# Kernel optimization log

Hardware: AMD Instinct MI355X
Metric: run time of the kernel (lower is better)

The kernel has to match this reference:

```python
import jax, jax.numpy as jnp
import numpy as np

H, S, B, R, IN, NN, OP = 512, 256, 32, 16, 4, 16, 6
NEG = -1.0e12


def setup_inputs() -> dict:
    key = jax.random.key(0)
    ks = jax.random.split(key, 40)
    f32 = jnp.float32
    inp = {}
    inp["node_emb"] = jax.random.normal(ks[0], (B, 1, H), f32)
    inp["left"] = jax.random.normal(ks[1], (B, 1, H), f32)
    inp["encoder_outputs"] = jax.random.normal(ks[2], (S, B, H), f32)
    inp["num_pades"] = jax.random.normal(ks[3], (B, NN, H), f32)
    inp["formula_scores"] = jax.random.normal(ks[4], (R, H), f32)
    inp["has_left"] = jax.random.bernoulli(ks[5], 0.5, (B,))
    lengths = jax.random.randint(ks[6], (B,), S // 2, S + 1)
    inp["seq_mask"] = jnp.arange(S)[None, :] >= lengths[:, None]
    nlen = jax.random.randint(ks[7], (B,), (IN + NN) // 2, IN + NN + 1)
    inp["mask_nums"] = jnp.arange(IN + NN)[None, :] >= nlen[:, None]
    sc = 0.04  # init scale for weights
    def w(i, shape):
        return jax.random.normal(ks[i], shape, f32) * sc
    inp["embedding_weight"] = jax.random.normal(ks[8], (1, IN, H), f32)
    inp["Wcl"] = w(9, (H, H));    inp["bcl"] = jnp.zeros((H,), f32)
    inp["Wclg"] = w(10, (H, H));  inp["bclg"] = jnp.zeros((H,), f32)
    inp["Wcr"] = w(11, (2 * H, H));  inp["bcr"] = jnp.zeros((H,), f32)
    inp["Wcrg"] = w(12, (2 * H, H)); inp["bcrg"] = jnp.zeros((H,), f32)
    inp["Wops"] = w(13, (2 * H, OP)); inp["bops"] = jnp.zeros((OP,), f32)
    inp["Wattn"] = w(14, (2 * H, H)); inp["battn"] = jnp.zeros((H,), f32)
    inp["wattn_s"] = w(15, (H,));     inp["battn_s"] = jnp.zeros((), f32)
    inp["Wfattn"] = w(16, (2 * H, H)); inp["bfattn"] = jnp.zeros((H,), f32)
    inp["wfattn_s"] = w(17, (H,));     inp["bfattn_s"] = jnp.zeros((), f32)
    inp["Wscore"] = w(18, (3 * H, H)); inp["bscore"] = jnp.zeros((H,), f32)
    inp["wscore_s"] = w(19, (H,))  # Score.score has no bias
    inp["Wfp1"] = w(20, (H, H));   inp["bfp1"] = jnp.zeros((H,), f32)
    inp["Wfp2"] = w(21, (H,));     inp["bfp2"] = jnp.zeros((), f32)
    return inp


def _forward(node_emb, left, has_left, encoder_outputs, num_pades, seq_mask,
             mask_nums, formula_scores, embedding_weight, Wcl, bcl, Wclg, bclg,
             Wcr, bcr, Wcrg, bcrg, Wops, bops, Wattn, battn, wattn_s, battn_s,
             Wfattn, bfattn, wfattn_s, bfattn_s, Wscore, bscore, wscore_s,
             Wfp1, bfp1, Wfp2, bfp2):
    # gated left/right node update (dropout = identity, eval mode)
    c = node_emb                                            # [B,1,H]
    lc = jnp.concatenate([left, c], axis=-1)                # [B,1,2H]
    out_l = jnp.tanh(c @ Wcl + bcl) * jax.nn.sigmoid(c @ Wclg + bclg)
    out_r = jnp.tanh(lc @ Wcr + bcr) * jax.nn.sigmoid(lc @ Wcrg + bcrg)
    current_node = jnp.where(has_left[:, None, None], out_r, out_l)  # [B,1,H]
    # TreeAttn(current_node, encoder_outputs): additive attention over S
    Wh, We = Wattn[:H], Wattn[H:]
    feat = jnp.tanh(current_node[:, 0][None] @ Wh + encoder_outputs @ We + battn)  # [S,B,H]
    en = (feat @ wattn_s + battn_s).T                       # [B,S]
    en = jnp.where(seq_mask, NEG, en)
    current_attn = jax.nn.softmax(en, axis=1)[:, None, :]   # [B,1,S]
    eo_b = jnp.transpose(encoder_outputs, (1, 0, 2))        # [B,S,H]
    current_context = current_attn @ eo_b                   # [B,1,H]
    # embedding table = learned constants + numbers from the problem
    emb_w = jnp.concatenate(
        [jnp.broadcast_to(embedding_weight, (node_emb.shape[0], IN, H)), num_pades], axis=1)  # [B,IN+NN,H]
    leaf_input = jnp.concatenate([current_node, current_context], axis=2)[:, 0]  # [B,2H]
    # FormulaAttn: additive attention of each formula over all tokens
    Wfe, Wff = Wfattn[:H], Wfattn[H:]
    ffeat = jnp.tanh(encoder_outputs[None] @ Wfe
                     + (formula_scores @ Wff)[:, None, None, :] + bfattn)  # [R,S,B,H]
    fen = jnp.transpose(ffeat @ wfattn_s + bfattn_s, (2, 0, 1))            # [B,R,S]
    fen = jnp.where(seq_mask[:, None, :], NEG, fen)
    formulas_attn = jax.nn.softmax(fen, axis=-1)            # [B,R,S]
    formulas_context = (formulas_attn + 0.2 * current_attn) @ eo_b         # [B,R,H]
    formula_feat = jnp.tanh(formulas_context @ Wfp1 + bfp1)
    formula_prob = jax.nn.softmax(formula_feat @ Wfp2 + bfp2, axis=-1)     # [B,R]
    # Score over candidate number embeddings
    N = IN + NN
    hid = jnp.broadcast_to(leaf_input[:, None, :], (leaf_input.shape[0], N, 2 * H))
    ein = jnp.concatenate([hid, emb_w], axis=-1)            # [B,N,3H]
    ns = jnp.tanh(ein @ Wscore + bscore) @ wscore_s         # [B,N]
    num_score = jnp.where(mask_nums, NEG, ns)
    op = leaf_input @ Wops + bops                           # [B,OP]
    return (num_score, op, current_node, current_context, emb_w, formula_prob)


def reference(node_emb, left, has_left, encoder_outputs, num_pades, seq_mask,
              mask_nums, formula_scores, embedding_weight, Wcl, bcl, Wclg, bclg,
              Wcr, bcr, Wcrg, bcrg, Wops, bops, Wattn, battn, wattn_s, battn_s,
              Wfattn, bfattn, wfattn_s, bfattn_s, Wscore, bscore, wscore_s,
              Wfp1, bfp1, Wfp2, bfp2):
    return _forward(node_emb, left, has_left, encoder_outputs, num_pades,
                    seq_mask, mask_nums, formula_scores, embedding_weight,
                    Wcl, bcl, Wclg, bclg, Wcr, bcr, Wcrg, bcrg, Wops, bops,
                    Wattn, battn, wattn_s, battn_s, Wfattn, bfattn, wfattn_s,
                    bfattn_s, Wscore, bscore, wscore_s, Wfp1, bfp1, Wfp2, bfp2)
```

## Files before the change

### kernel.cpp

```cpp
#include <hip/hip_runtime.h>
#include <hip/hip_bf16.h>
#include <stdint.h>

#define H 512
#define S 256
#define B 32
#define R 16
#define NEG -1000000000000.0f

typedef unsigned short u16;
typedef short short8 __attribute__((ext_vector_type(8)));
typedef float f32x4 __attribute__((ext_vector_type(4)));

__device__ __forceinline__ float bf2f(u16 u) {
  unsigned int v = ((unsigned int)u) << 16;
  float f; __builtin_memcpy(&f, &v, 4); return f;
}
__device__ __forceinline__ u16 f2u(float x) {
  __hip_bfloat16 h = __float2bfloat16(x);
  u16 u; __builtin_memcpy(&u, &h, 2); return u;
}
__device__ __forceinline__ float ftanh(float x) {
  float e = __expf(2.f * x);
  return 1.f - 2.f * __builtin_amdgcn_rcpf(e + 1.f);
}
__device__ __forceinline__ float fsig(float x) {
  return __builtin_amdgcn_rcpf(1.f + __expf(-x));
}
__device__ __forceinline__ void gload16(const void* g, void* l) {
  __builtin_amdgcn_global_load_lds(
      (const __attribute__((address_space(1))) unsigned int*)g,
      (__attribute__((address_space(3))) unsigned int*)l, 16, 0, 0);
}

__device__ __forceinline__ void trans_tile(const float* __restrict__ src, int nb, int k0,
                                           u16* __restrict__ dst, int n0, int Krows,
                                           float (*tile)[65], int t) {
  #pragma unroll
  for (int it = 0; it < 16; ++it) {
    int f = it * 256 + t; int r = f >> 6, c = f & 63;
    tile[r][c] = src[(size_t)(k0 + r) * 512 + nb + c];
  }
  __syncthreads();
  #pragma unroll
  for (int it = 0; it < 16; ++it) {
    int f = it * 256 + t; int r = f >> 6, c = f & 63;
    dst[(size_t)(n0 + r) * Krows + k0 + c] = f2u(tile[c][r]);
  }
}

__global__ __launch_bounds__(256) void k_prep1(
    const float* __restrict__ enc, u16* __restrict__ encb,
    const float* __restrict__ Wattn, const float* __restrict__ Wfattn, u16* __restrict__ Wt,
    const float* __restrict__ Wscore, u16* __restrict__ Wt2f,
    const float* __restrict__ Wfp1, u16* __restrict__ Wt3,
    const float* __restrict__ node_emb, const float* __restrict__ left,
    const int* __restrict__ has_left,
    const float* __restrict__ Wcl, const float* __restrict__ Wclg,
    const float* __restrict__ Wcr, const float* __restrict__ Wcrg,
    const float* __restrict__ fs,
    float* __restrict__ gp1, float* __restrict__ gp2, float* __restrict__ cwp,
    const float* __restrict__ emb_w, const float* __restrict__ num_pades,
    float* __restrict__ out_embw, u16* __restrict__ einb) {
  __shared__ float tile[64][65];
  __shared__ float x[128];
  int id = blockIdx.x, t = threadIdx.x;
  if (id < 2048) {
    int i = (id * 256 + t) * 8;
    float4 a = *(const float4*)(enc + i);
    float4 b = *(const float4*)(enc + i + 4);
    short8 o;
    o[0] = (short)f2u(a.x); o[1] = (short)f2u(a.y); o[2] = (short)f2u(a.z); o[3] = (short)f2u(a.w);
    o[4] = (short)f2u(b.x); o[5] = (short)f2u(b.y); o[6] = (short)f2u(b.z); o[7] = (short)f2u(b.w);
    *(short8*)(encb + i) = o;
  } else if (id < 2176) {
    int f = id - 2048; int gx = f & 15, gy = f >> 4;
    int n0 = gx * 64, k0 = gy * 64;
    const float* src = (n0 < 512) ? (Wattn + 512 * 512) : Wfattn;
    int nb = (n0 < 512) ? n0 : n0 - 512;
    trans_tile(src, nb, k0, Wt, n0, 512, tile, t);
  } else if (id < 2368) {
    int f = id - 2176; int gx = f & 7, gy = f >> 3;
    trans_tile(Wscore, gx * 64, gy * 64, Wt2f, gx * 64, 1536, tile, t);
  } else if (id < 2432) {
    int f = id - 2368; int gx = f & 7, gy = f >> 3;
    trans_tile(Wfp1, gx * 64, gy * 64, Wt3, gx * 64, 512, tile, t);
  } else if (id < 2688) {
    int f = id - 2432;
    int b = f >> 3, kc = f & 7;
    int hl = has_left[b];
    int k0 = kc * 128;
    float* o1 = gp1 + ((size_t)b * 8 + kc) * 512;
    float* o2 = gp2 + ((size_t)b * 8 + kc) * 512;
    if (!hl && kc >= 4) { o1[t] = 0.f; o1[t + 256] = 0.f; o2[t] = 0.f; o2[t + 256] = 0.f; return; }
    if (t < 128) {
      int k = k0 + t;
      x[t] = hl ? (k < 512 ? left[b * 512 + k] : node_emb[b * 512 + k - 512])
                : node_emb[b * 512 + k];
    }
    __syncthreads();
    const float* W1 = hl ? Wcr : Wcl;
    const float* W2 = hl ? Wcrg : Wclg;
    float a1 = 0.f, a2 = 0.f, a3 = 0.f, a4 = 0.f;
    for (int kk = 0; kk < 128; ++kk) {
      float xv = x[kk];
      const float* w1r = W1 + (size_t)(k0 + kk) * 512;
      const float* w2r = W2 + (size_t)(k0 + kk) * 512;
      a1 += xv * w1r[t]; a2 += xv * w1r[t + 256];
      a3 += xv * w2r[t]; a4 += xv * w2r[t + 256];
    }
    o1[t] = a1; o1[t + 256] = a2; o2[t] = a3; o2[t + 256] = a4;
  } else if (id < 2752) {
    int f = id - 2688; int row = f >> 2, kc = f & 3;
    int k0 = kc * 128;
    if (t < 128) x[t] = fs[row * 512 + k0 + t];
    __syncthreads();
    const float* W = Wfattn + (size_t)(512 + k0) * 512;
    float a1 = 0.f, a2 = 0.f;
    for (int kk = 0; kk < 128; ++kk) {
      float xv = x[kk];
      a1 += xv * W[(size_t)kk * 512 + t];
      a2 += xv * W[(size_t)kk * 512 + t + 256];
    }
    float* o = cwp + ((size_t)(32 + row) * 4 + kc) * 512;
    o[t] = a1; o[t + 256] = a2;
  } else {
    int f = id - 2752;
    #pragma unroll
    for (int rr = 0; rr < 2; ++rr) {
      int row = f * 2 + rr;
      int n = row % 20, b = row / 20;
      #pragma unroll
      for (int i = 0; i < 2; ++i) {
        int h = t + 256 * i;
        float v = (n < 4) ? emb_w[n * 512 + h] : num_pades[((size_t)b * 16 + n - 4) * 512 + h];
        out_embw[(size_t)row * 512 + h] = v;
        einb[(size_t)row * 1536 + 1024 + h] = f2u(v);
      }
    }
  }
}

template <int FM, int FN, bool OUT16>
__device__ __forceinline__ void gemm_body(
    const u16* __restrict__ A, const u16* __restrict__ Bt,
    u16* __restrict__ C16, float* __restrict__ C32,
    int lda, int ldb, int ldc, int ksteps,
    int bm, int bn, int kbase, long zoff,
    u16* As, u16* Bs) {
  constexpr int BM = FM * 32, BN = FN * 32;
  const int tid = threadIdx.x;
  const int lane = tid & 63;
  const int wid = tid >> 6;
  const int wr = (wid >> 1) * (FM * 16);
  const int wc = (wid & 1) * (FN * 16);
  f32x4 acc[FM][FN];
  #pragma unroll
  for (int m = 0; m < FM; ++m)
    #pragma unroll
    for (int n = 0; n < FN; ++n)
      #pragma unroll
      for (int q = 0; q < 4; ++q) acc[m][n][q] = 0.f;

  const int kb = (lane >> 4) * 8;
  const int rr = lane & 15;
  for (int ks = 0; ks < ksteps; ++ks) {
    int k0 = kbase + ks * 32;
    #pragma unroll
    for (int it = 0; it < BM / 64; ++it) {
      int c = it * 256 + tid;
      gload16(A + (size_t)(bm + (c >> 2)) * lda + k0 + (c & 3) * 8, As + c * 8);
    }
    #pragma unroll
    for (int it = 0; it < BN / 64; ++it) {
      int c = it * 256 + tid;
      gload16(Bt + (size_t)(bn + (c >> 2)) * ldb + k0 + (c & 3) * 8, Bs + c * 8);
    }
    __syncthreads();
    short8 af[FM], bf[FN];
    #pragma unroll
    for (int m = 0; m < FM; ++m)
      af[m] = *(const short8*)(As + (wr + m * 16 + rr) * 32 + kb);
    #pragma unroll
    for (int n = 0; n < FN; ++n)
      bf[n] = *(const short8*)(Bs + (wc + n * 16 + rr) * 32 + kb);
    #pragma unroll
    for (int m = 0; m < FM; ++m)
      #pragma unroll
      for (int n = 0; n < FN; ++n)
        acc[m][n] = __builtin_amdgcn_mfma_f32_16x16x32_bf16(af[m], bf[n], acc[m][n], 0, 0, 0);
    __syncthreads();
  }
  int r0 = (lane >> 4) * 4, cc = lane & 15;
  #pragma unroll
  for (int m = 0; m < FM; ++m)
    #pragma unroll
    for (int n = 0; n < FN; ++n)
      #pragma unroll
      for (int q = 0; q < 4; ++q) {
        long row = bm + wr + m * 16 + r0 + q;
        long col = bn + wc + n * 16 + cc;
        if (OUT16) C16[zoff + row * ldc + col] = f2u(acc[m][n][q]);
        else       C32[zoff + row * ldc + col] = acc[m][n][q];
      }
}

__global__ __launch_bounds__(256) void k_g1(
    const u16* __restrict__ encb, const u16* __restrict__ Wt, u16* __restrict__ EW,
    const float* __restrict__ cwp, const float* __restrict__ battn,
    const float* __restrict__ bfattn, float* __restrict__ CW, float* __restrict__ FW) {
  __shared__ u16 As[128 * 32];
  __shared__ u16 Bs[128 * 32];
  if (blockIdx.y == 0 && blockIdx.x < 48) {
    int row = blockIdx.x, t = threadIdx.x;
    #pragma unroll
    for (int i = 0; i < 2; ++i) {
      int h = t + 256 * i;
      float s = cwp[((size_t)row * 4 + 0) * 512 + h] + cwp[((size_t)row * 4 + 1) * 512 + h] +
                cwp[((size_t)row * 4 + 2) * 512 + h] + cwp[((size_t)row * 4 + 3) * 512 + h];
      if (row < 32) CW[row * 512 + h] = s + battn[h];
      else          FW[(row - 32) * 512 + h] = s + bfattn[h];
    }
  }
  gemm_body<4, 4, true>(encb, Wt, EW, nullptr, 512, 512, 1024, 16,
                        blockIdx.x * 128, blockIdx.y * 128, 0, 0, As, Bs);
}

__global__ __launch_bounds__(256) void k_tt(
    const u16* __restrict__ einb, const u16* __restrict__ Wt2f, float* __restrict__ Tp,
    const u16* __restrict__ fctxb, const u16* __restrict__ Wt3, float* __restrict__ T3p) {
  __shared__ u16 As[64 * 32];
  __shared__ u16 Bs[64 * 32];
  int q = blockIdx.x;
  if (q < 320) {
    int x = q % 10, y = (q / 10) % 8, z = q / 80;
    gemm_body<2, 2, false>(einb, Wt2f, nullptr, Tp, 1536, 1536, 512, 12,
                           x * 64, y * 64, z * 12 * 32, (long)z * 327680, As, Bs);
  } else {
    int q2 = q - 320;
    int x = q2 % 8, y = (q2 / 8) % 8, z = q2 / 64;
    gemm_body<2, 2, false>(fctxb, Wt3, nullptr, T3p, 512, 512, 512, 8,
                           x * 64, y * 64, z * 8 * 32, (long)z * 262144, As, Bs);
  }
}

__global__ __launch_bounds__(256) void k_p2(
    const float* __restrict__ gp1, const float* __restrict__ gp2,
    const int* __restrict__ has_left,
    const float* __restrict__ bcl, const float* __restrict__ bclg,
    const float* __restrict__ bcr, const float* __restrict__ bcrg,
    const float* __restrict__ Wattn,
    float* __restrict__ cur_node, float* __restrict__ out_cn, float* __restrict__ cwp) {
  int id = blockIdx.x, t = threadIdx.x;
  int row = id >> 2, kc = id & 3;
  int k0 = kc * 128;
  __shared__ float x[128];
  int hl = has_left[row];
  if (t < 128) {
    int h = k0 + t;
    float s1 = 0.f, s2 = 0.f;
    #pragma unroll
    for (int c = 0; c < 8; ++c) {
      s1 += gp1[((size_t)row * 8 + c) * 512 + h];
      s2 += gp2[((size_t)row * 8 + c) * 512 + h];
    }
    float v = ftanh(s1 + (hl ? bcr[h] : bcl[h])) * fsig(s2 + (hl ? bcrg[h] : bclg[h]));
    x[t] = v;
    cur_node[row * 512 + h] = v;
    out_cn[row * 512 + h] = v;
  }
  __syncthreads();
  const float* W = Wattn + (size_t)k0 * 512;
  float a1 = 0.f, a2 = 0.f;
  for (int kk = 0; kk < 128; ++kk) {
    float xv = x[kk];
    a1 += xv * W[(size_t)kk * 512 + t];
    a2 += xv * W[(size_t)kk * 512 + t + 256];
  }
  float* o = cwp + ((size_t)row * 4 + kc) * 512;
  o[t] = a1; o[t + 256] = a2;
}

__global__ __launch_bounds__(256) void k_enfen(
    const u16* __restrict__ EW, const float* __restrict__ CW,
    const float* __restrict__ FW,
    const float* __restrict__ wattn_s, const float* __restrict__ battn_s,
    const float* __restrict__ wfattn_s, const float* __restrict__ bfattn_s,
    const int* __restrict__ seq_mask, float* __restrict__ en, float* __restrict__ fen) {
  __shared__ float sFW[16 * 512];
  __shared__ float swf[512], swa[512], scw[512];
  int bid = blockIdx.x;
  int b = bid >> 6;
  int s0 = (bid & 63) * 4;
  int t = threadIdx.x;
  #pragma unroll
  for (int q = 0; q < 32; ++q) sFW[q * 256 + t] = FW[q * 256 + t];
  swf[t] = wfattn_s[t]; swf[256 + t] = wfattn_s[256 + t];
  swa[t] = wattn_s[t];  swa[256 + t] = wattn_s[256 + t];
  scw[t] = CW[b * 512 + t]; scw[256 + t] = CW[b * 512 + 256 + t];
  __syncthreads();
  int w = t >> 6, lane = t & 63;
  int s = s0 + w;
  const u16* ew = EW + (size_t)(s * 32 + b) * 1024;
  float ewf[8], wfv[8];
  float accE = 0.f;
  #pragma unroll
  for (int i = 0; i < 8; ++i) {
    int h = lane + 64 * i;
    accE += ftanh(scw[h] + bf2f(ew[h])) * swa[h];
    ewf[i] = bf2f(ew[512 + h]);
    wfv[i] = swf[h];
  }
  for (int o = 32; o >= 1; o >>= 1) accE += __shfl_down(accE, o);
  int msk = seq_mask[b * 256 + s];
  if (lane == 0) en[b * 256 + s] = msk ? NEG : (accE + battn_s[0]);
  for (int r = 0; r < 16; ++r) {
    float a = 0.f;
    #pragma unroll
    for (int i = 0; i < 8; ++i) {
      int h = lane + 64 * i;
      a += ftanh(sFW[r * 512 + h] + ewf[i]) * wfv[i];
    }
    for (int o = 32; o >= 1; o >>= 1) a += __shfl_down(a, o);
    if (lane == 0) fen[((size_t)b * 16 + r) * 256 + s] = msk ? NEG : (a + bfattn_s[0]);
  }
}

__global__ __launch_bounds__(512) void k_ctxall(
    const float* __restrict__ en, const float* __restrict__ fen,
    const u16* __restrict__ encb, const float* __restrict__ cur_node,
    float* __restrict__ out_ctx, float* __restrict__ leaf, u16* __restrict__ fctxb,
    u16* __restrict__ einb) {
  int br = blockIdx.x;
  int b = br / 17, j = br % 17;
  int t = threadIdx.x;
  __shared__ float red[512];
  __shared__ float sa[256];
  float xe = (t < 256) ? en[b * 256 + t] : NEG;
  red[t] = xe; __syncthreads();
  for (int o = 256; o > 0; o >>= 1) { if (t < o) red[t] = fmaxf(red[t], red[t + o]); __syncthreads(); }
  float m = red[0]; __syncthreads();
  float ee = (t < 256) ? __expf(xe - m) : 0.f;
  red[t] = ee; __syncthreads();
  for (int o = 256; o > 0; o >>= 1) { if (t < o) red[t] += red[t + o]; __syncthreads(); }
  float attn_v = ee / red[0];
  __syncthreads();
  float coef = attn_v;
  if (j < 16) {
    float xf = (t < 256) ? fen[((size_t)b * 16 + j) * 256 + t] : NEG;
    red[t] = xf; __syncthreads();
    for (int o = 256; o > 0; o >>= 1) { if (t < o) red[t] = fmaxf(red[t], red[t + o]); __syncthreads(); }
    float mf = red[0]; __syncthreads();
    float ef = (t < 256) ? __expf(xf - mf) : 0.f;
    red[t] = ef; __syncthreads();
    for (int o = 256; o > 0; o >>= 1) { if (t < o) red[t] += red[t + o]; __syncthreads(); }
    coef = ef / red[0] + 0.2f * attn_v;
    __syncthreads();
  }
  if (t < 256) sa[t] = coef;
  __syncthreads();
  int h = t;
  float acc = 0.f;
  for (int s = 0; s < 256; ++s)
    acc += sa[s] * bf2f(encb[((size_t)s * 32 + b) * 512 + h]);
  if (j < 16) {
    fctxb[((size_t)b * 16 + j) * 512 + h] = f2u(acc);
  } else {
    float cn = cur_node[b * 512 + h];
    out_ctx[b * 512 + h] = acc;
    leaf[b * 1024 + 512 + h] = acc;
    leaf[b * 1024 + h] = cn;
    u16 v1 = f2u(cn), v2 = f2u(acc);
    for (int n = 0; n < 20; ++n) {
      einb[(size_t)(b * 20 + n) * 1536 + h] = v1;
      einb[(size_t)(b * 20 + n) * 1536 + 512 + h] = v2;
    }
  }
}

__global__ __launch_bounds__(256) void k_epi(
    const float* __restrict__ Tp, const float* __restrict__ bscore,
    const float* __restrict__ wscore_s, const int* __restrict__ mask_nums,
    float* __restrict__ out_ns,
    const float* __restrict__ T3p, const float* __restrict__ bfp1,
    const float* __restrict__ Wfp2, const float* __restrict__ bfp2,
    float* __restrict__ out_fp,
    const float* __restrict__ leaf, const float* __restrict__ Wops,
    const float* __restrict__ bops, float* __restrict__ out_op) {
  int id = blockIdx.x, t = threadIdx.x;
  int w = t >> 6, lane = t & 63;
  __shared__ float red[16];
  if (id < 640) {
    int row = id;
    float acc = 0.f;
    #pragma unroll
    for (int i = 0; i < 2; ++i) {
      int h = t + 256 * i;
      float tv = Tp[(size_t)row * 512 + h] + Tp[327680 + (size_t)row * 512 + h] +
                 Tp[2L * 327680 + (size_t)row * 512 + h] + Tp[3L * 327680 + (size_t)row * 512 + h] +
                 bscore[h];
      acc += ftanh(tv) * wscore_s[h];
    }
    for (int o = 32; o >= 1; o >>= 1) acc += __shfl_down(acc, o);
    if (lane == 0) red[w] = acc;
    __syncthreads();
    if (t == 0) out_ns[row] = mask_nums[row] ? NEG : (red[0] + red[1] + red[2] + red[3]);
  } else if (id < 672) {
    int b = id - 640;
    #pragma unroll
    for (int j2 = 0; j2 < 4; ++j2) {
      int j = w * 4 + j2;
      int row = b * 16 + j;
      float acc = 0.f;
      #pragma unroll
      for (int i = 0; i < 8; ++i) {
        int h = lane + 64 * i;
        float v = T3p[(size_t)row * 512 + h] + T3p[262144 + (size_t)row * 512 + h] + bfp1[h];
        acc += ftanh(v) * Wfp2[h];
      }
      for (int o = 32; o >= 1; o >>= 1) acc += __shfl_down(acc, o);
      if (lane == 0) red[j] = acc + bfp2[0];
    }
    __syncthreads();
    if (t < 16) {
      float xx = red[t];
      float mm = xx;
      for (int o = 8; o >= 1; o >>= 1) mm = fmaxf(mm, __shfl_xor(mm, o, 16));
      float e = __expf(xx - mm);
      float s2 = e;
      for (int o = 8; o >= 1; o >>= 1) s2 += __shfl_xor(s2, o, 16);
      out_fp[b * 16 + t] = e / s2;
    }
  } else {
    int f = id - 672; int o = f % 6, b = f / 6;
    float acc = 0.f;
    #pragma unroll
    for (int i = 0; i < 4; ++i) {
      int k = t + 256 * i;
      acc += leaf[b * 1024 + k] * Wops[(size_t)k * 6 + o];
    }
    for (int off = 32; off >= 1; off >>= 1) acc += __shfl_down(acc, off);
    if (lane == 0) red[w] = acc;
    __syncthreads();
    if (t == 0) out_op[b * 6 + o] = red[0] + red[1] + red[2] + red[3] + bops[o];
  }
}

extern "C" void kernel_launch(void* const* d_in, const int* in_sizes, int n_in,
                              void* d_out, int out_size, void* d_ws, size_t ws_size,
                              hipStream_t stream) {
  const float* node_emb  = (const float*)d_in[0];
  const float* left      = (const float*)d_in[1];
  const float* enc       = (const float*)d_in[2];
  const float* num_pades = (const float*)d_in[3];
  const float* fs        = (const float*)d_in[4];
  const int*   has_left  = (const int*)d_in[5];
  const int*   seq_mask  = (const int*)d_in[6];
  const int*   mask_nums = (const int*)d_in[7];
  const float* emb_w     = (const float*)d_in[8];
  const float* Wcl  = (const float*)d_in[9];
  const float* bcl  = (const float*)d_in[10];
  const float* Wclg = (const float*)d_in[11];
  const float* bclg = (const float*)d_in[12];
  const float* Wcr  = (const float*)d_in[13];
  const float* bcr  = (const float*)d_in[14];
  const float* Wcrg = (const float*)d_in[15];
  const float* bcrg = (const float*)d_in[16];
  const float* Wops = (const float*)d_in[17];
  const float* bops = (const float*)d_in[18];
  const float* Wattn   = (const float*)d_in[19];
  const float* battn   = (const float*)d_in[20];
  const float* wattn_s = (const float*)d_in[21];
  const float* battn_s = (const float*)d_in[22];
  const float* Wfattn   = (const float*)d_in[23];
  const float* bfattn   = (const float*)d_in[24];
  const float* wfattn_s = (const float*)d_in[25];
  const float* bfattn_s = (const float*)d_in[26];
  const float* Wscore   = (const float*)d_in[27];
  const float* bscore   = (const float*)d_in[28];
  const float* wscore_s = (const float*)d_in[29];
  const float* Wfp1 = (const float*)d_in[30];
  const float* bfp1 = (const float*)d_in[31];
  const float* Wfp2 = (const float*)d_in[32];
  const float* bfp2 = (const float*)d_in[33];

  float* out = (float*)d_out;
  float* out_ns   = out + 0;
  float* out_op   = out + 640;
  float* out_cn   = out + 832;
  float* out_ctx  = out + 17216;
  float* out_embw = out + 33600;
  float* out_fp   = out + 361280;

  uint8_t* wsb = (uint8_t*)d_ws;
  u16*   encb = (u16*)(wsb + 0);
  u16*   Wt   = (u16*)(wsb + 8388608);
  u16*   Wt2f = (u16*)(wsb + 9437184);
  u16*   Wt3  = (u16*)(wsb + 11010048);
  u16*   EW   = (u16*)(wsb + 11534336);
  u16*   einb = (u16*)(wsb + 28311552);
  float* Tp   = (float*)(wsb + 30277632);
  float* T3p  = (float*)(wsb + 35520512);
  float* fb   = (float*)(wsb + 37617664);
  float* cur_node = fb + 0;
  float* CW   = fb + 16384;
  float* FW   = fb + 32768;
  float* en   = fb + 40960;
  float* fen  = fb + 49152;
  float* leaf = fb + 180224;
  u16*   fctxb= (u16*)(fb + 212992);
  float* gp1  = fb + 344064;
  float* gp2  = fb + 475136;
  float* cwp  = fb + 606208;

  k_prep1<<<3072, 256, 0, stream>>>(enc, encb, Wattn, Wfattn, Wt, Wscore, Wt2f, Wfp1, Wt3,
                                    node_emb, left, has_left, Wcl, Wclg, Wcr, Wcrg, fs,
                                    gp1, gp2, cwp, emb_w, num_pades, out_embw, einb);
  k_p2<<<128, 256, 0, stream>>>(gp1, gp2, has_left, bcl, bclg, bcr, bcrg, Wattn,
                                cur_node, out_cn, cwp);
  k_g1<<<dim3(64, 8), 256, 0, stream>>>(encb, Wt, EW, cwp, battn, bfattn, CW, FW);
  k_enfen<<<2048, 256, 0, stream>>>(EW, CW, FW, wattn_s, battn_s, wfattn_s, bfattn_s, seq_mask, en, fen);
  k_ctxall<<<544, 512, 0, stream>>>(en, fen, encb, cur_node, out_ctx, leaf, fctxb, einb);
  k_tt<<<448, 256, 0, stream>>>(einb, Wt2f, Tp, fctxb, Wt3, T3p);
  k_epi<<<864, 256, 0, stream>>>(Tp, bscore, wscore_s, mask_nums, out_ns,
                                 T3p, bfp1, Wfp2, bfp2, out_fp,
                                 leaf, Wops, bops, out_op);
}
```

Before: 118.0 us.

## Move attention projections into MFMA GEMM and deepen split-K for score GEMMs

The current_node@Wattn and formula_scores@Wfattn projections, previously scalar fp32 matvecs in k_prep1/k_p2, are now a bf16 MFMA GEMM tile added to k_g1 using a newly transposed weight Wt4. Biases are folded into k_enfen. The split-K factor of the k_tt GEMMs doubles to raise block count, and the epilogue sums more partials. It also unrolls the context loop. The cost is an extra weight transpose, more partial-sum traffic, and bf16 rounding of the projection inputs.

```diff
diff --git a/kernel.cpp b/kernel.cpp
--- a/kernel.cpp
+++ b/kernel.cpp
@@ -54,12 +54,12 @@
     const float* __restrict__ Wattn, const float* __restrict__ Wfattn, u16* __restrict__ Wt,
     const float* __restrict__ Wscore, u16* __restrict__ Wt2f,
     const float* __restrict__ Wfp1, u16* __restrict__ Wt3,
+    u16* __restrict__ Wt4,
     const float* __restrict__ node_emb, const float* __restrict__ left,
     const int* __restrict__ has_left,
     const float* __restrict__ Wcl, const float* __restrict__ Wclg,
     const float* __restrict__ Wcr, const float* __restrict__ Wcrg,
-    const float* __restrict__ fs,
-    float* __restrict__ gp1, float* __restrict__ gp2, float* __restrict__ cwp,
+    float* __restrict__ gp1, float* __restrict__ gp2,
     const float* __restrict__ emb_w, const float* __restrict__ num_pades,
     float* __restrict__ out_embw, u16* __restrict__ einb) {
   __shared__ float tile[64][65];
@@ -85,8 +85,14 @@
   } else if (id < 2432) {
     int f = id - 2368; int gx = f & 7, gy = f >> 3;
     trans_tile(Wfp1, gx * 64, gy * 64, Wt3, gx * 64, 512, tile, t);
-  } else if (id < 2688) {
-    int f = id - 2432;
+  } else if (id < 2560) {
+    int f = id - 2432; int gx = f & 15, gy = f >> 4;
+    int n0 = gx * 64, k0 = gy * 64;
+    const float* src = (n0 < 512) ? Wattn : (Wfattn + 512 * 512);
+    int nb = (n0 < 512) ? n0 : n0 - 512;
+    trans_tile(src, nb, k0, Wt4, n0, 512, tile, t);
+  } else if (id < 2816) {
+    int f = id - 2560;
     int b = f >> 3, kc = f & 7;
     int hl = has_left[b];
     int k0 = kc * 128;
@@ -110,22 +116,8 @@
       a3 += xv * w2r[t]; a4 += xv * w2r[t + 256];
     }
     o1[t] = a1; o1[t + 256] = a2; o2[t] = a3; o2[t + 256] = a4;
-  } else if (id < 2752) {
-    int f = id - 2688; int row = f >> 2, kc = f & 3;
-    int k0 = kc * 128;
-    if (t < 128) x[t] = fs[row * 512 + k0 + t];
-    __syncthreads();
-    const float* W = Wfattn + (size_t)(512 + k0) * 512;
-    float a1 = 0.f, a2 = 0.f;
-    for (int kk = 0; kk < 128; ++kk) {
-      float xv = x[kk];
-      a1 += xv * W[(size_t)kk * 512 + t];
-      a2 += xv * W[(size_t)kk * 512 + t + 256];
-    }
-    float* o = cwp + ((size_t)(32 + row) * 4 + kc) * 512;
-    o[t] = a1; o[t + 256] = a2;
   } else {
-    int f = id - 2752;
+    int f = id - 2816;
     #pragma unroll
     for (int rr = 0; rr < 2; ++rr) {
       int row = f * 2 + rr;
@@ -141,7 +133,7 @@
   }
 }
 
-template <int FM, int FN, bool OUT16>
+template <int FM, int FN>
 __device__ __forceinline__ void gemm_body(
     const u16* __restrict__ A, const u16* __restrict__ Bt,
     u16* __restrict__ C16, float* __restrict__ C32,
@@ -200,30 +192,21 @@
       for (int q = 0; q < 4; ++q) {
         long row = bm + wr + m * 16 + r0 + q;
         long col = bn + wc + n * 16 + cc;
-        if (OUT16) C16[zoff + row * ldc + col] = f2u(acc[m][n][q]);
-        else       C32[zoff + row * ldc + col] = acc[m][n][q];
+        if (C16) C16[zoff + row * ldc + col] = f2u(acc[m][n][q]);
+        else     C32[zoff + row * ldc + col] = acc[m][n][q];
       }
 }
 
 __global__ __launch_bounds__(256) void k_g1(
     const u16* __restrict__ encb, const u16* __restrict__ Wt, u16* __restrict__ EW,
-    const float* __restrict__ cwp, const float* __restrict__ battn,
-    const float* __restrict__ bfattn, float* __restrict__ CW, float* __restrict__ FW) {
+    const u16* __restrict__ cnfs, const u16* __restrict__ Wt4, float* __restrict__ CWFW) {
   __shared__ u16 As[128 * 32];
   __shared__ u16 Bs[128 * 32];
-  if (blockIdx.y == 0 && blockIdx.x < 48) {
-    int row = blockIdx.x, t = threadIdx.x;
-    #pragma unroll
-    for (int i = 0; i < 2; ++i) {
-      int h = t + 256 * i;
-      float s = cwp[((size_t)row * 4 + 0) * 512 + h] + cwp[((size_t)row * 4 + 1) * 512 + h] +
-                cwp[((size_t)row * 4 + 2) * 512 + h] + cwp[((size_t)row * 4 + 3) * 512 + h];
-      if (row < 32) CW[row * 512 + h] = s + battn[h];
-      else          FW[(row - 32) * 512 + h] = s + bfattn[h];
-    }
-  }
-  gemm_body<4, 4, true>(encb, Wt, EW, nullptr, 512, 512, 1024, 16,
-                        blockIdx.x * 128, blockIdx.y * 128, 0, 0, As, Bs);
+  int x = blockIdx.x, y = blockIdx.y;
+  if (x < 64)
+    gemm_body<4, 4>(encb, Wt, EW, nullptr, 512, 512, 1024, 16, x * 128, y * 128, 0, 0, As, Bs);
+  else
+    gemm_body<4, 4>(cnfs, Wt4, nullptr, CWFW, 512, 512, 1024, 16, 0, y * 128, 0, 0, As, Bs);
 }
 
 __global__ __launch_bounds__(256) void k_tt(
@@ -232,15 +215,15 @@
   __shared__ u16 As[64 * 32];
   __shared__ u16 Bs[64 * 32];
   int q = blockIdx.x;
-  if (q < 320) {
+  if (q < 640) {
     int x = q % 10, y = (q / 10) % 8, z = q / 80;
-    gemm_body<2, 2, false>(einb, Wt2f, nullptr, Tp, 1536, 1536, 512, 12,
-                           x * 64, y * 64, z * 12 * 32, (long)z * 327680, As, Bs);
+    gemm_body<2, 2>(einb, Wt2f, nullptr, Tp, 1536, 1536, 512, 6,
+                    x * 64, y * 64, z * 6 * 32, (long)z * 327680, As, Bs);
   } else {
-    int q2 = q - 320;
+    int q2 = q - 640;
     int x = q2 % 8, y = (q2 / 8) % 8, z = q2 / 64;
-    gemm_body<2, 2, false>(fctxb, Wt3, nullptr, T3p, 512, 512, 512, 8,
-                           x * 64, y * 64, z * 8 * 32, (long)z * 262144, As, Bs);
+    gemm_body<2, 2>(fctxb, Wt3, nullptr, T3p, 512, 512, 512, 4,
+                    x * 64, y * 64, z * 4 * 32, (long)z * 262144, As, Bs);
   }
 }
 
@@ -249,41 +232,41 @@
     const int* __restrict__ has_left,
     const float* __restrict__ bcl, const float* __restrict__ bclg,
     const float* __restrict__ bcr, const float* __restrict__ bcrg,
-    const float* __restrict__ Wattn,
-    float* __restrict__ cur_node, float* __restrict__ out_cn, float* __restrict__ cwp) {
+    const float* __restrict__ fs,
+    float* __restrict__ cur_node, float* __restrict__ out_cn, u16* __restrict__ cnfs) {
   int id = blockIdx.x, t = threadIdx.x;
-  int row = id >> 2, kc = id & 3;
-  int k0 = kc * 128;
-  __shared__ float x[128];
-  int hl = has_left[row];
-  if (t < 128) {
-    int h = k0 + t;
-    float s1 = 0.f, s2 = 0.f;
-    #pragma unroll
-    for (int c = 0; c < 8; ++c) {
-      s1 += gp1[((size_t)row * 8 + c) * 512 + h];
-      s2 += gp2[((size_t)row * 8 + c) * 512 + h];
-    }
-    float v = ftanh(s1 + (hl ? bcr[h] : bcl[h])) * fsig(s2 + (hl ? bcrg[h] : bclg[h]));
-    x[t] = v;
-    cur_node[row * 512 + h] = v;
-    out_cn[row * 512 + h] = v;
-  }
-  __syncthreads();
-  const float* W = Wattn + (size_t)k0 * 512;
-  float a1 = 0.f, a2 = 0.f;
-  for (int kk = 0; kk < 128; ++kk) {
-    float xv = x[kk];
-    a1 += xv * W[(size_t)kk * 512 + t];
-    a2 += xv * W[(size_t)kk * 512 + t + 256];
-  }
-  float* o = cwp + ((size_t)row * 4 + kc) * 512;
-  o[t] = a1; o[t + 256] = a2;
+  if (id < 32) {
+    int b = id, hl = has_left[b];
+    #pragma unroll
+    for (int i = 0; i < 2; ++i) {
+      int h = t + 256 * i;
+      float s1 = 0.f, s2 = 0.f;
+      #pragma unroll
+      for (int c = 0; c < 8; ++c) {
+        s1 += gp1[((size_t)b * 8 + c) * 512 + h];
+        s2 += gp2[((size_t)b * 8 + c) * 512 + h];
+      }
+      float v = ftanh(s1 + (hl ? bcr[h] : bcl[h])) * fsig(s2 + (hl ? bcrg[h] : bclg[h]));
+      cur_node[b * 512 + h] = v;
+      out_cn[b * 512 + h] = v;
+      cnfs[b * 512 + h] = f2u(v);
+    }
+  } else if (id < 48) {
+    int r = id - 32;
+    #pragma unroll
+    for (int i = 0; i < 2; ++i) {
+      int h = t + 256 * i;
+      cnfs[id * 512 + h] = f2u(fs[r * 512 + h]);
+    }
+  } else {
+    #pragma unroll
+    for (int i = 0; i < 2; ++i) cnfs[id * 512 + t + 256 * i] = 0;
+  }
 }
 
 __global__ __launch_bounds__(256) void k_enfen(
-    const u16* __restrict__ EW, const float* __restrict__ CW,
-    const float* __restrict__ FW,
+    const u16* __restrict__ EW, const float* __restrict__ CWFW,
+    const float* __restrict__ battn, const float* __restrict__ bfattn,
     const float* __restrict__ wattn_s, const float* __restrict__ battn_s,
     const float* __restrict__ wfattn_s, const float* __restrict__ bfattn_s,
     const int* __restrict__ seq_mask, float* __restrict__ en, float* __restrict__ fen) {
@@ -294,10 +277,15 @@
   int s0 = (bid & 63) * 4;
   int t = threadIdx.x;
   #pragma unroll
-  for (int q = 0; q < 32; ++q) sFW[q * 256 + t] = FW[q * 256 + t];
+  for (int q = 0; q < 32; ++q) {
+    int flat = q * 256 + t;
+    int r = flat >> 9, h = flat & 511;
+    sFW[flat] = CWFW[(size_t)(32 + r) * 1024 + 512 + h] + bfattn[h];
+  }
   swf[t] = wfattn_s[t]; swf[256 + t] = wfattn_s[256 + t];
   swa[t] = wattn_s[t];  swa[256 + t] = wattn_s[256 + t];
-  scw[t] = CW[b * 512 + t]; scw[256 + t] = CW[b * 512 + 256 + t];
+  scw[t] = CWFW[(size_t)b * 1024 + t] + battn[t];
+  scw[256 + t] = CWFW[(size_t)b * 1024 + 256 + t] + battn[256 + t];
   __syncthreads();
   int w = t >> 6, lane = t & 63;
   int s = s0 + w;
@@ -361,6 +349,7 @@
   __syncthreads();
   int h = t;
   float acc = 0.f;
+  #pragma unroll 8
   for (int s = 0; s < 256; ++s)
     acc += sa[s] * bf2f(encb[((size_t)s * 32 + b) * 512 + h]);
   if (j < 16) {
@@ -396,9 +385,9 @@
     #pragma unroll
     for (int i = 0; i < 2; ++i) {
       int h = t + 256 * i;
-      float tv = Tp[(size_t)row * 512 + h] + Tp[327680 + (size_t)row * 512 + h] +
-                 Tp[2L * 327680 + (size_t)row * 512 + h] + Tp[3L * 327680 + (size_t)row * 512 + h] +
-                 bscore[h];
+      float tv = bscore[h];
+      #pragma unroll
+      for (int z = 0; z < 8; ++z) tv += Tp[(size_t)z * 327680 + (size_t)row * 512 + h];
       acc += ftanh(tv) * wscore_s[h];
     }
     for (int o = 32; o >= 1; o >>= 1) acc += __shfl_down(acc, o);
@@ -415,7 +404,9 @@
       #pragma unroll
       for (int i = 0; i < 8; ++i) {
         int h = lane + 64 * i;
-        float v = T3p[(size_t)row * 512 + h] + T3p[262144 + (size_t)row * 512 + h] + bfp1[h];
+        float v = bfp1[h];
+        #pragma unroll
+        for (int z = 0; z < 4; ++z) v += T3p[(size_t)z * 262144 + (size_t)row * 512 + h];
         acc += ftanh(v) * Wfp2[h];
       }
       for (int o = 32; o >= 1; o >>= 1) acc += __shfl_down(acc, o);
@@ -497,31 +488,32 @@
   u16*   Wt   = (u16*)(wsb + 8388608);
   u16*   Wt2f = (u16*)(wsb + 9437184);
   u16*   Wt3  = (u16*)(wsb + 11010048);
-  u16*   EW   = (u16*)(wsb + 11534336);
-  u16*   einb = (u16*)(wsb + 28311552);
-  float* Tp   = (float*)(wsb + 30277632);
-  float* T3p  = (float*)(wsb + 35520512);
-  float* fb   = (float*)(wsb + 37617664);
+  u16*   Wt4  = (u16*)(wsb + 11534336);
+  u16*   EW   = (u16*)(wsb + 12582912);
+  u16*   einb = (u16*)(wsb + 29360128);
+  u16*   cnfs = (u16*)(wsb + 31326208);
+  float* CWFW = (float*)(wsb + 31457280);
+  float* Tp   = (float*)(wsb + 31981568);
+  float* T3p  = (float*)(wsb + 42467328);
+  float* fb   = (float*)(wsb + 46661632);
   float* cur_node = fb + 0;
-  float* CW   = fb + 16384;
-  float* FW   = fb + 32768;
-  float* en   = fb + 40960;
-  float* fen  = fb + 49152;
-  float* leaf = fb + 180224;
-  u16*   fctxb= (u16*)(fb + 212992);
-  float* gp1  = fb + 344064;
-  float* gp2  = fb + 475136;
-  float* cwp  = fb + 606208;
-
-  k_prep1<<<3072, 256, 0, stream>>>(enc, encb, Wattn, Wfattn, Wt, Wscore, Wt2f, Wfp1, Wt3,
-                                    node_emb, left, has_left, Wcl, Wclg, Wcr, Wcrg, fs,
-                                    gp1, gp2, cwp, emb_w, num_pades, out_embw, einb);
-  k_p2<<<128, 256, 0, stream>>>(gp1, gp2, has_left, bcl, bclg, bcr, bcrg, Wattn,
-                                cur_node, out_cn, cwp);
-  k_g1<<<dim3(64, 8), 256, 0, stream>>>(encb, Wt, EW, cwp, battn, bfattn, CW, FW);
-  k_enfen<<<2048, 256, 0, stream>>>(EW, CW, FW, wattn_s, battn_s, wfattn_s, bfattn_s, seq_mask, en, fen);
+  float* en   = fb + 16384;
+  float* fen  = fb + 24576;
+  float* leaf = fb + 155648;
+  u16*   fctxb= (u16*)(fb + 188416);
+  float* gp1  = fb + 319488;
+  float* gp2  = fb + 450560;
+
+  k_prep1<<<3136, 256, 0, stream>>>(enc, encb, Wattn, Wfattn, Wt, Wscore, Wt2f, Wfp1, Wt3, Wt4,
+                                    node_emb, left, has_left, Wcl, Wclg, Wcr, Wcrg,
+                                    gp1, gp2, emb_w, num_pades, out_embw, einb);
+  k_p2<<<128, 256, 0, stream>>>(gp1, gp2, has_left, bcl, bclg, bcr, bcrg, fs,
+                                cur_node, out_cn, cnfs);
+  k_g1<<<dim3(65, 8), 256, 0, stream>>>(encb, Wt, EW, cnfs, Wt4, CWFW);
+  k_enfen<<<2048, 256, 0, stream>>>(EW, CWFW, battn, bfattn, wattn_s, battn_s,
+                                    wfattn_s, bfattn_s, seq_mask, en, fen);
   k_ctxall<<<544, 512, 0, stream>>>(en, fen, encb, cur_node, out_ctx, leaf, fctxb, einb);
-  k_tt<<<448, 256, 0, stream>>>(einb, Wt2f, Tp, fctxb, Wt3, T3p);
+  k_tt<<<896, 256, 0, stream>>>(einb, Wt2f, Tp, fctxb, Wt3, T3p);
   k_epi<<<864, 256, 0, stream>>>(Tp, bscore, wscore_s, mask_nums, out_ns,
                                  T3p, bfp1, Wfp2, bfp2, out_fp,
                                  leaf, Wops, bops, out_op);
```

After: 115.7 us. About the same (-1.9%).
